# Performance work log

Hardware: AMD Instinct MI355X
Metric: run time of the kernel (lower is better)

Reference implementation:

```python
import jax, jax.numpy as jnp
import numpy as np

E, H, KVH, S, N = 2048, 16, 4, 4096, 1
D = E // H            # head_dim = 128
G = H // KVH          # groups = 4
KV_DIM = KVH * D


def setup_inputs() -> dict:
    key = jax.random.key(0)
    ks = jax.random.split(key, 7)
    sc = 0.02
    seq = jax.random.normal(ks[0], (N, S, E), dtype=jnp.float32)
    # causal mask, 0 = masked (matches masked_fill(mask == 0, -inf))
    mask = jnp.tril(jnp.ones((S, S), dtype=jnp.int32))[None, None]  # [1,1,S,S]
    return {
        "seq": seq,
        "mask": mask,
        "Wq_w": jax.random.normal(ks[1], (E, E), dtype=jnp.float32) * sc,
        "Wq_b": jnp.zeros((E,), dtype=jnp.float32),
        "Wkv_w": jax.random.normal(ks[2], (2 * KV_DIM, E), dtype=jnp.float32) * sc,
        "Wkv_b": jnp.zeros((2 * KV_DIM,), dtype=jnp.float32),
        "Wo_w": jax.random.normal(ks[3], (E, E), dtype=jnp.float32) * sc,
        "Wo_b": jnp.zeros((E,), dtype=jnp.float32),
    }


def reference(seq, mask, Wq_w, Wq_b, Wkv_w, Wkv_b, Wo_w, Wo_b):
    n, s, _ = seq.shape
    q = seq @ Wq_w.T + Wq_b                      # [N,S,E]
    kv = seq @ Wkv_w.T + Wkv_b                   # [N,S,2*KV_DIM]
    Q = q.reshape(n, s, H, D).transpose(0, 2, 1, 3)         # [N,H,S,D]
    KV = kv.reshape(n, s, 2, KVH, D)
    K = KV[:, :, 0].transpose(0, 2, 1, 3)                   # [N,KVH,S,D]
    V = KV[:, :, 1].transpose(0, 2, 1, 3)                   # [N,KVH,S,D]
    # repeat_interleave over head dim (GQA expansion)
    Kr = jnp.repeat(K, G, axis=1)                           # [N,H,S,D]
    Vr = jnp.repeat(V, G, axis=1)
    energy = jnp.einsum("nhqd,nhkd->nhqk", Q, Kr)           # [N,H,S,S]
    neg = jnp.finfo(energy.dtype).min
    energy = jnp.where(mask == 0, neg, energy)
    attn = jax.nn.softmax(energy / jnp.sqrt(jnp.float32(D)), axis=3)
    out = jnp.einsum("nhqk,nhkd->nhqd", attn, Vr)           # [N,H,S,D]
    out = out.transpose(0, 2, 1, 3).reshape(n, s, E)
    out = out @ Wo_w.T + Wo_b
    return out, K, V
```

## Files before the change

### kernel.cpp

```cpp
#include <hip/hip_runtime.h>
#include <cstdint>
#include <cstddef>

typedef __bf16 bf16_t;
typedef __bf16 bf16x8 __attribute__((ext_vector_type(8)));
typedef float  f32x4  __attribute__((ext_vector_type(4)));
typedef float  f32x16 __attribute__((ext_vector_type(16)));
typedef unsigned int u32x4 __attribute__((ext_vector_type(4)));

#define LDQ 3072

__global__ __launch_bounds__(256)
void cast_kernel(const float* __restrict__ in, bf16_t* __restrict__ out, int n8) {
  int i = blockIdx.x * 256 + threadIdx.x;
  if (i >= n8) return;
  const float4* p = reinterpret_cast<const float4*>(in) + (size_t)i * 2;
  float4 a = p[0], b = p[1];
  bf16x8 o;
  o[0] = (bf16_t)a.x; o[1] = (bf16_t)a.y; o[2] = (bf16_t)a.z; o[3] = (bf16_t)a.w;
  o[4] = (bf16_t)b.x; o[5] = (bf16_t)b.y; o[6] = (bf16_t)b.z; o[7] = (bf16_t)b.w;
  *reinterpret_cast<bf16x8*>(out + (size_t)i * 8) = o;
}

template <int MODE>
__global__ __launch_bounds__(256, 3)
void gemm128(const bf16_t* __restrict__ A, const bf16_t* __restrict__ B,
             const float* __restrict__ bias0, const float* __restrict__ bias1,
             void* __restrict__ out0, float* __restrict__ kvout,
             bf16_t* __restrict__ vt, int M, int N, int K) {
  __shared__ __align__(16) char smem[32768];
  const int t = threadIdx.x;
  const int l = t & 63;
  const int lr = l & 15, lh = l >> 4;
  const int w = t >> 6;
  const int wm = w >> 1, wn = w & 1;
  const int m0 = blockIdx.x * 128, n0 = blockIdx.y * 128;

  const char* Ag = (const char*)(A + (size_t)m0 * K);
  const char* Bg = (const char*)(B + (size_t)n0 * K);

#define STAGE_U(dst, src, ks)                                                   \
  { _Pragma("unroll")                                                           \
    for (int p = 0; p < 2; ++p) {                                               \
      int c = p * 256 + t;                                                      \
      int row = c >> 2;                                                         \
      int c16 = (c & 3) ^ ((row >> 1) & 3);                                     \
      __builtin_amdgcn_global_load_lds(                                         \
        (const __attribute__((address_space(1))) void*)                         \
          ((src) + (size_t)row * (size_t)(K * 2) + (size_t)(ks) * 64 + c16 * 16), \
        (__attribute__((address_space(3))) void*)((dst) + c * 16), 16, 0, 0);   \
    } }

  f32x4 acc[4][4] = {};
  bf16x8 a[4], b[4];
  char* const s0 = smem;
  char* const s1 = smem + 16384;

#define RD_B(base)                                                              \
  { _Pragma("unroll")                                                           \
    for (int j = 0; j < 4; ++j) {                                               \
      int row = wn * 64 + j * 16 + lr;                                          \
      b[j] = *reinterpret_cast<const bf16x8*>(                                  \
          (base) + 8192 + row * 64 + ((lh ^ ((row >> 1) & 3)) << 4));           \
    } }
#define RD_A2(base, i0)                                                         \
  { _Pragma("unroll")                                                           \
    for (int ii = 0; ii < 2; ++ii) {                                            \
      int row = wm * 64 + ((i0) + ii) * 16 + lr;                                \
      a[(i0) + ii] = *reinterpret_cast<const bf16x8*>(                          \
          (base) + row * 64 + ((lh ^ ((row >> 1) & 3)) << 4));                  \
    } }
#define MFMA8(i0)                                                               \
  asm volatile("s_waitcnt lgkmcnt(0)" ::: "memory");                            \
  __builtin_amdgcn_sched_barrier(0);                                            \
  __builtin_amdgcn_s_setprio(1);                                                \
  { _Pragma("unroll")                                                           \
    for (int ii = 0; ii < 2; ++ii)                                              \
      _Pragma("unroll")                                                         \
      for (int j = 0; j < 4; ++j)                                               \
        acc[(i0) + ii][j] =                                                     \
          __builtin_amdgcn_mfma_f32_16x16x32_bf16(a[(i0)+ii], b[j], acc[(i0)+ii][j], 0, 0, 0); } \
  __builtin_amdgcn_s_setprio(0);                                                \
  __builtin_amdgcn_sched_barrier(0);
#define BAR  __builtin_amdgcn_s_barrier(); __builtin_amdgcn_sched_barrier(0);

  const int NK = K >> 5;
  STAGE_U(s0, Ag, 0);
  STAGE_U(s0 + 8192, Bg, 0);

  for (int it2 = 0; it2 < (NK >> 1); ++it2) {
    const int k1 = 2 * it2 + 1, k2 = 2 * it2 + 2;
    STAGE_U(s1, Ag, k1);
    asm volatile("s_waitcnt vmcnt(2)" ::: "memory");
    BAR;
    RD_B(s0); RD_A2(s0, 0);
    MFMA8(0);
    BAR;
    RD_A2(s0, 2);
    STAGE_U(s1 + 8192, Bg, k1);
    MFMA8(2);
    BAR;
    if (k2 < NK) {
      STAGE_U(s0, Ag, k2);
      asm volatile("s_waitcnt vmcnt(2)" ::: "memory");
    } else {
      asm volatile("s_waitcnt vmcnt(0)" ::: "memory");
    }
    BAR;
    RD_B(s1); RD_A2(s1, 0);
    MFMA8(0);
    BAR;
    RD_A2(s1, 2);
    if (k2 < NK) STAGE_U(s0 + 8192, Bg, k2);
    MFMA8(2);
    BAR;
  }
#undef STAGE_U
#undef RD_A2
#undef RD_B
#undef MFMA8
#undef BAR

  #pragma unroll
  for (int j = 0; j < 4; ++j) {
    const int col = n0 + wn * 64 + j * 16 + lr;
    float bv;
    if constexpr (MODE == 0) bv = bias0[col];
    else bv = (col < 2048) ? bias0[col] : bias1[col - 2048];
    #pragma unroll
    for (int i = 0; i < 4; ++i) {
      #pragma unroll
      for (int r = 0; r < 4; ++r) {
        const int row = m0 + wm * 64 + i * 16 + lh * 4 + r;
        float v = acc[i][j][r] + bv;
        if constexpr (MODE == 0) {
          reinterpret_cast<float*>(out0)[(size_t)row * N + col] = v;
        } else {
          float qv = (col < 2048) ? v * 0.1275187541f : v;
          reinterpret_cast<bf16_t*>(out0)[(size_t)row * N + col] = (bf16_t)qv;
          if (col >= 2048) {
            const int local = col - 2048;
            const int which = local >> 9;
            const int hd    = local & 511;
            kvout[(size_t)which * 2097152 +
                  ((size_t)(hd >> 7) * 4096 + row) * 128 + (hd & 127)] = v;
            if (local >= 512) {
              const int c2 = local - 512;
              vt[(size_t)(c2 >> 7) * 524288 + (size_t)(c2 & 127) * 4096 + row] = (bf16_t)v;
            }
          }
        }
      }
    }
  }
}

__global__ __launch_bounds__(256, 2)
void attn_kernel(const bf16_t* __restrict__ QKVb, const bf16_t* __restrict__ Vt,
                 bf16_t* __restrict__ Ob) {
  __shared__ __align__(16) char smem[65536];
  const int t = threadIdx.x;
  const int w = t >> 6, l = t & 63;
  const int q5 = l & 31, hi = l >> 5;
  const int g = w >> 1;
  const int wq = w & 1;
  const int h = blockIdx.y, kvh = h >> 2;

  const char* Kg = (const char*)(QKVb + 2048 + (size_t)kvh * 128);
  const char* Vg = (const char*)(Vt + (size_t)kvh * 524288);

#define STAGE_K(buf, kv0)                                                          \
  {                                                                                \
    _Pragma("unroll")                                                              \
    for (int p = 0; p < 4; ++p) {                                                  \
      int chunk = p * 256 + t;                                                     \
      int row = chunk >> 4, cb = (chunk & 15) << 4;                                \
      __builtin_amdgcn_global_load_lds(                                            \
        (const __attribute__((address_space(1))) void*)                            \
            (Kg + (size_t)((kv0) + row) * 6144 + (cb ^ ((row & 7) << 4))),         \
        (__attribute__((address_space(3))) void*)(smem + (buf) * 16384 + chunk * 16),\
        16, 0, 0);                                                                 \
    }                                                                              \
  }
#define STAGE_V(buf, kv0)                                                          \
  {                                                                                \
    _Pragma("unroll")                                                              \
    for (int p = 0; p < 4; ++p) {                                                  \
      int chunk = p * 256 + t;                                                     \
      int row = chunk >> 3, cb = (chunk & 7) << 4;                                 \
      __builtin_amdgcn_global_load_lds(                                            \
        (const __attribute__((address_space(1))) void*)                            \
            (Vg + (size_t)row * 8192 + (size_t)(kv0) * 2 + (cb ^ ((row & 7) << 4))),\
        (__attribute__((address_space(3))) void*)(smem + 32768 + (buf) * 16384 + chunk * 16),\
        16, 0, 0);                                                                 \
    }                                                                              \
  }
#define CROW(r) (((r) & 3) + 8 * ((r) >> 2) + 4 * hi)

  bf16x8 onesf;
  #pragma unroll
  for (int j = 0; j < 8; ++j) onesf[j] = (bf16_t)1.0f;

  for (int ph = 0; ph < 2; ++ph) {
    const int xt = ph ? 63 - (int)blockIdx.x : (int)blockIdx.x;
    const int q0w = xt * 64 + wq * 32;
    const int nIter = xt + 1;

    bf16x8 qf[8];
    {
      const bf16_t* qp = QKVb + (size_t)(q0w + q5) * LDQ + h * 128 + hi * 8;
      #pragma unroll
      for (int kc = 0; kc < 8; ++kc) qf[kc] = *reinterpret_cast<const bf16x8*>(qp + kc * 16);
    }
    __builtin_amdgcn_sched_barrier(0);
    STAGE_K(0, 0);
    STAGE_V(0, 0);
    __builtin_amdgcn_sched_barrier(0);
    STAGE_K(1, 64);
    STAGE_V(1, 64);
    __builtin_amdgcn_sched_barrier(0);

    f32x16 oacc[4] = {};
    f32x16 lacc = {};

    auto body = [&](int it, bool masked) {
      const int cur = it & 1;
      const int kv0 = it * 64;
      if (it + 1 < nIter) { asm volatile("s_waitcnt vmcnt(8)" ::: "memory"); }
      else                { asm volatile("s_waitcnt vmcnt(0)" ::: "memory"); }
      __builtin_amdgcn_s_barrier();
      __builtin_amdgcn_sched_barrier(0);

      const int krow = g * 32 + q5;
      const char* ka = smem + cur * 16384 + krow * 256;
      const int ksw = (krow & 7) << 4;
      f32x16 s = {};
      __builtin_amdgcn_s_setprio(1);
      #pragma unroll
      for (int kc = 0; kc < 8; ++kc) {
        bf16x8 kf = *reinterpret_cast<const bf16x8*>(ka + ((kc * 32 + hi * 16) ^ ksw));
        s = __builtin_amdgcn_mfma_f32_32x32x16_bf16(kf, qf[kc], s, 0, 0, 0);
      }
      __builtin_amdgcn_s_setprio(0);

      float e_[16];
      #pragma unroll
      for (int r = 0; r < 16; ++r) {
        float p = exp2f(s[r]);
        if (masked && (kv0 + g * 32 + CROW(r) > q0w + q5)) p = 0.f;
        e_[r] = p;
      }
      unsigned int pk_[8];
      #pragma unroll
      for (int pr = 0; pr < 8; ++pr) {
        unsigned int wrd;
        asm("v_cvt_pk_bf16_f32 %0, %1, %2" : "=v"(wrd) : "v"(e_[2 * pr]), "v"(e_[2 * pr + 1]));
        pk_[pr] = wrd;
      }
      asm("v_permlane32_swap_b32 %0, %1" : "+v"(pk_[0]), "+v"(pk_[2]));
      asm("v_permlane32_swap_b32 %0, %1" : "+v"(pk_[1]), "+v"(pk_[3]));
      asm("v_permlane32_swap_b32 %0, %1" : "+v"(pk_[4]), "+v"(pk_[6]));
      asm("v_permlane32_swap_b32 %0, %1" : "+v"(pk_[5]), "+v"(pk_[7]));
      u32x4 pw0 = {pk_[0], pk_[1], pk_[2], pk_[3]};
      u32x4 pw1 = {pk_[4], pk_[5], pk_[6], pk_[7]};
      bf16x8 pa0 = *reinterpret_cast<bf16x8*>(&pw0);
      bf16x8 pa1 = *reinterpret_cast<bf16x8*>(&pw1);

      lacc = __builtin_amdgcn_mfma_f32_32x32x16_bf16(pa0, onesf, lacc, 0, 0, 0);
      lacc = __builtin_amdgcn_mfma_f32_32x32x16_bf16(pa1, onesf, lacc, 0, 0, 0);

      const char* vb0 = smem + 32768 + cur * 16384;
      __builtin_amdgcn_s_setprio(1);
      #pragma unroll
      for (int db = 0; db < 4; ++db) {
        const int vrow = db * 32 + q5;
        const char* va = vb0 + vrow * 128;
        const int vsw = (vrow & 7) << 4;
        bf16x8 v0 = *reinterpret_cast<const bf16x8*>(va + ((g * 64 + hi * 16) ^ vsw));
        bf16x8 v1 = *reinterpret_cast<const bf16x8*>(va + ((g * 64 + 32 + hi * 16) ^ vsw));
        oacc[db] = __builtin_amdgcn_mfma_f32_32x32x16_bf16(pa0, v0, oacc[db], 0, 0, 0);
        oacc[db] = __builtin_amdgcn_mfma_f32_32x32x16_bf16(pa1, v1, oacc[db], 0, 0, 0);
      }
      __builtin_amdgcn_s_setprio(0);

      __builtin_amdgcn_sched_barrier(0);
      __builtin_amdgcn_s_barrier();
      __builtin_amdgcn_sched_barrier(0);
      if (it + 2 < nIter) { STAGE_K(cur, kv0 + 128); STAGE_V(cur, kv0 + 128); }
    };

    for (int it = 0; it < nIter - 1; ++it) body(it, false);
    body(nIter - 1, true);

    bf16_t* mO = (bf16_t*)smem;
    float*  mL = (float*)(smem + 32768);
    if (g == 1) {
      #pragma unroll
      for (int db = 0; db < 4; ++db)
        #pragma unroll
        for (int r = 0; r < 16; ++r)
          mO[(wq * 32 + CROW(r)) * 128 + db * 32 + q5] = (bf16_t)oacc[db][r];
      if (q5 == 0)
        #pragma unroll
        for (int r = 0; r < 16; ++r) mL[wq * 32 + CROW(r)] = lacc[r];
    }
    __syncthreads();
    if (g == 0) {
      float linv[16];
      #pragma unroll
      for (int r = 0; r < 16; ++r)
        linv[r] = 1.0f / (lacc[r] + mL[wq * 32 + CROW(r)]);
      #pragma unroll
      for (int db = 0; db < 4; ++db) {
        #pragma unroll
        for (int r = 0; r < 16; ++r) {
          float o1 = (float)mO[(wq * 32 + CROW(r)) * 128 + db * 32 + q5];
          float v = (oacc[db][r] + o1) * linv[r];
          Ob[(size_t)(q0w + CROW(r)) * 2048 + h * 128 + db * 32 + q5] = (bf16_t)v;
        }
      }
    }
    __syncthreads();
  }
#undef STAGE_K
#undef STAGE_V
#undef CROW
}

extern "C" void kernel_launch(void* const* d_in, const int* in_sizes, int n_in,
                              void* d_out, int out_size, void* d_ws, size_t ws_size,
                              hipStream_t stream) {
  const float* seq   = (const float*)d_in[0];
  const float* Wq_w  = (const float*)d_in[2];
  const float* Wq_b  = (const float*)d_in[3];
  const float* Wkv_w = (const float*)d_in[4];
  const float* Wkv_b = (const float*)d_in[5];
  const float* Wo_w  = (const float*)d_in[6];
  const float* Wo_b  = (const float*)d_in[7];

  float* out   = (float*)d_out;
  float* kvout = out + (size_t)4096 * 2048;

  char* ws = (char*)d_ws;
  bf16_t* seqb = (bf16_t*)ws;
  bf16_t* wqkv = (bf16_t*)(ws + 16777216);
  bf16_t* wob  = (bf16_t*)(ws + 29360128);
  bf16_t* qkvb = (bf16_t*)(ws + 37748736);
  bf16_t* vt   = (bf16_t*)(ws + 62914560);
  bf16_t* ob   = seqb;

  cast_kernel<<<4096, 256, 0, stream>>>(seq, seqb, 1048576);
  cast_kernel<<<2048, 256, 0, stream>>>(Wq_w, wqkv, 524288);
  cast_kernel<<<1024, 256, 0, stream>>>(Wkv_w, wqkv + 4194304, 262144);
  cast_kernel<<<2048, 256, 0, stream>>>(Wo_w, wob, 524288);

  gemm128<1><<<dim3(32, 24), 256, 0, stream>>>(seqb, wqkv, Wq_b, Wkv_b,
                                               qkvb, kvout, vt, 4096, 3072, 2048);
  attn_kernel<<<dim3(32, 16), 256, 0, stream>>>(qkvb, vt, ob);
  gemm128<0><<<dim3(32, 16), 256, 0, stream>>>(ob, wob, Wo_b, nullptr,
                                               out, nullptr, nullptr, 4096, 2048, 2048);
}
```

Before: 231.3 us.

## Load K/V tiles directly into registers instead of double-buffered LDS staging

Replaces the double-buffered global_load_lds staging of K and V tiles with direct per-wave global loads into register fragments, prefetching the next tile after each MFMA phase. Shared memory shrinks to just the epilogue merge buffer, and the per-iteration block barriers disappear. The cost is that each wave pair loads K/V redundantly from global/L2 with less coalesced access (V rows strided by 8192 bytes), and register pressure rises, which may hurt occupancy.

```diff
diff --git a/kernel.cpp b/kernel.cpp
--- a/kernel.cpp
+++ b/kernel.cpp
@@ -158,7 +158,7 @@
 __global__ __launch_bounds__(256, 2)
 void attn_kernel(const bf16_t* __restrict__ QKVb, const bf16_t* __restrict__ Vt,
                  bf16_t* __restrict__ Ob) {
-  __shared__ __align__(16) char smem[65536];
+  __shared__ __align__(16) char smem[16640];
   const int t = threadIdx.x;
   const int w = t >> 6, l = t & 63;
   const int q5 = l & 31, hi = l >> 5;
@@ -169,33 +169,19 @@
   const char* Kg = (const char*)(QKVb + 2048 + (size_t)kvh * 128);
   const char* Vg = (const char*)(Vt + (size_t)kvh * 524288);
 
-#define STAGE_K(buf, kv0)                                                          \
-  {                                                                                \
-    _Pragma("unroll")                                                              \
-    for (int p = 0; p < 4; ++p) {                                                  \
-      int chunk = p * 256 + t;                                                     \
-      int row = chunk >> 4, cb = (chunk & 15) << 4;                                \
-      __builtin_amdgcn_global_load_lds(                                            \
-        (const __attribute__((address_space(1))) void*)                            \
-            (Kg + (size_t)((kv0) + row) * 6144 + (cb ^ ((row & 7) << 4))),         \
-        (__attribute__((address_space(3))) void*)(smem + (buf) * 16384 + chunk * 16),\
-        16, 0, 0);                                                                 \
-    }                                                                              \
-  }
-#define STAGE_V(buf, kv0)                                                          \
-  {                                                                                \
-    _Pragma("unroll")                                                              \
-    for (int p = 0; p < 4; ++p) {                                                  \
-      int chunk = p * 256 + t;                                                     \
-      int row = chunk >> 3, cb = (chunk & 7) << 4;                                 \
-      __builtin_amdgcn_global_load_lds(                                            \
-        (const __attribute__((address_space(1))) void*)                            \
-            (Vg + (size_t)row * 8192 + (size_t)(kv0) * 2 + (cb ^ ((row & 7) << 4))),\
-        (__attribute__((address_space(3))) void*)(smem + 32768 + (buf) * 16384 + chunk * 16),\
-        16, 0, 0);                                                                 \
-    }                                                                              \
-  }
 #define CROW(r) (((r) & 3) + 8 * ((r) >> 2) + 4 * hi)
+#define LOADK(ka, kv0)                                                          \
+  { const char* kr_ = Kg + (size_t)((kv0) + g * 32 + q5) * 6144 + hi * 16;      \
+    _Pragma("unroll")                                                           \
+    for (int kc = 0; kc < 8; ++kc)                                              \
+      ka[kc] = *reinterpret_cast<const bf16x8*>(kr_ + kc * 32); }
+#define LOADV(va, kv0)                                                          \
+  { _Pragma("unroll")                                                           \
+    for (int db = 0; db < 4; ++db) {                                            \
+      const char* vr_ = Vg + (size_t)(db * 32 + q5) * 8192 +                    \
+                        (size_t)(kv0) * 2 + g * 64 + hi * 16;                   \
+      va[db * 2]     = *reinterpret_cast<const bf16x8*>(vr_);                   \
+      va[db * 2 + 1] = *reinterpret_cast<const bf16x8*>(vr_ + 32); } }
 
   bf16x8 onesf;
   #pragma unroll
@@ -212,36 +198,27 @@
       #pragma unroll
       for (int kc = 0; kc < 8; ++kc) qf[kc] = *reinterpret_cast<const bf16x8*>(qp + kc * 16);
     }
-    __builtin_amdgcn_sched_barrier(0);
-    STAGE_K(0, 0);
-    STAGE_V(0, 0);
-    __builtin_amdgcn_sched_barrier(0);
-    STAGE_K(1, 64);
-    STAGE_V(1, 64);
-    __builtin_amdgcn_sched_barrier(0);
+
+    bf16x8 ka[8], va[8];
+    LOADK(ka, 0);
+    LOADV(va, 0);
 
     f32x16 oacc[4] = {};
     f32x16 lacc = {};
 
     auto body = [&](int it, bool masked) {
-      const int cur = it & 1;
       const int kv0 = it * 64;
-      if (it + 1 < nIter) { asm volatile("s_waitcnt vmcnt(8)" ::: "memory"); }
-      else                { asm volatile("s_waitcnt vmcnt(0)" ::: "memory"); }
-      __builtin_amdgcn_s_barrier();
-      __builtin_amdgcn_sched_barrier(0);
-
-      const int krow = g * 32 + q5;
-      const char* ka = smem + cur * 16384 + krow * 256;
-      const int ksw = (krow & 7) << 4;
+
       f32x16 s = {};
       __builtin_amdgcn_s_setprio(1);
       #pragma unroll
-      for (int kc = 0; kc < 8; ++kc) {
-        bf16x8 kf = *reinterpret_cast<const bf16x8*>(ka + ((kc * 32 + hi * 16) ^ ksw));
-        s = __builtin_amdgcn_mfma_f32_32x32x16_bf16(kf, qf[kc], s, 0, 0, 0);
-      }
+      for (int kc = 0; kc < 8; ++kc)
+        s = __builtin_amdgcn_mfma_f32_32x32x16_bf16(ka[kc], qf[kc], s, 0, 0, 0);
       __builtin_amdgcn_s_setprio(0);
+
+      __builtin_amdgcn_sched_barrier(0);
+      if (it + 1 < nIter) LOADK(ka, kv0 + 64);
+      __builtin_amdgcn_sched_barrier(0);
 
       float e_[16];
       #pragma unroll
@@ -269,31 +246,24 @@
       lacc = __builtin_amdgcn_mfma_f32_32x32x16_bf16(pa0, onesf, lacc, 0, 0, 0);
       lacc = __builtin_amdgcn_mfma_f32_32x32x16_bf16(pa1, onesf, lacc, 0, 0, 0);
 
-      const char* vb0 = smem + 32768 + cur * 16384;
       __builtin_amdgcn_s_setprio(1);
       #pragma unroll
       for (int db = 0; db < 4; ++db) {
-        const int vrow = db * 32 + q5;
-        const char* va = vb0 + vrow * 128;
-        const int vsw = (vrow & 7) << 4;
-        bf16x8 v0 = *reinterpret_cast<const bf16x8*>(va + ((g * 64 + hi * 16) ^ vsw));
-        bf16x8 v1 = *reinterpret_cast<const bf16x8*>(va + ((g * 64 + 32 + hi * 16) ^ vsw));
-        oacc[db] = __builtin_amdgcn_mfma_f32_32x32x16_bf16(pa0, v0, oacc[db], 0, 0, 0);
-        oacc[db] = __builtin_amdgcn_mfma_f32_32x32x16_bf16(pa1, v1, oacc[db], 0, 0, 0);
+        oacc[db] = __builtin_amdgcn_mfma_f32_32x32x16_bf16(pa0, va[db * 2],     oacc[db], 0, 0, 0);
+        oacc[db] = __builtin_amdgcn_mfma_f32_32x32x16_bf16(pa1, va[db * 2 + 1], oacc[db], 0, 0, 0);
       }
       __builtin_amdgcn_s_setprio(0);
 
       __builtin_amdgcn_sched_barrier(0);
-      __builtin_amdgcn_s_barrier();
+      if (it + 1 < nIter) LOADV(va, kv0 + 64);
       __builtin_amdgcn_sched_barrier(0);
-      if (it + 2 < nIter) { STAGE_K(cur, kv0 + 128); STAGE_V(cur, kv0 + 128); }
     };
 
     for (int it = 0; it < nIter - 1; ++it) body(it, false);
     body(nIter - 1, true);
 
     bf16_t* mO = (bf16_t*)smem;
-    float*  mL = (float*)(smem + 32768);
+    float*  mL = (float*)(smem + 16384);
     if (g == 1) {
       #pragma unroll
       for (int db = 0; db < 4; ++db)
@@ -322,8 +292,8 @@
     }
     __syncthreads();
   }
-#undef STAGE_K
-#undef STAGE_V
+#undef LOADK
+#undef LOADV
 #undef CROW
 }
 
```

Result: slower. 380.1 us (+64.4%).
